# Performance work log

Measured on AMD Instinct MI355X. Metric: run time of the kernel, lower is better.

## Reference

```python
import jax, jax.numpy as jnp
import numpy as np
import math

H = W = 512
N_ANGLES = 180
TOTAL_ANGLES = 180.0
DIAG = int(math.ceil(math.sqrt(2.0) * max(H, W)))  # 725
PW = (DIAG - W) // 2  # 106
PH = (DIAG - H) // 2  # 106
P = W + 2 * PW        # 724 (torch F.pad arithmetic)


def setup_inputs() -> dict:
    key = jax.random.key(0)
    x = jax.random.normal(key, (H, W), dtype=jnp.float32)
    return {"x": x}


def _bilinear_sample_zeros(img, ix, iy):
    """grid_sample(align_corners=False, padding_mode='zeros') on a single [P,P] img.
    ix, iy: [N,P,P] pixel-space sample coords. Returns [N,P,P]."""
    n = img.shape[0]
    x0 = jnp.floor(ix)
    y0 = jnp.floor(iy)
    wx = ix - x0
    wy = iy - y0
    x0i = x0.astype(jnp.int32)
    y0i = y0.astype(jnp.int32)
    x1i = x0i + 1
    y1i = y0i + 1

    def g(yi, xi):
        v = img[jnp.clip(yi, 0, n - 1), jnp.clip(xi, 0, n - 1)]
        m = (yi >= 0) & (yi < n) & (xi >= 0) & (xi < n)
        return v * m.astype(img.dtype)

    return (g(y0i, x0i) * (1 - wx) * (1 - wy)
            + g(y0i, x1i) * wx * (1 - wy)
            + g(y1i, x0i) * (1 - wx) * wy
            + g(y1i, x1i) * wx * wy)


def reference(x):
    # pad image to (near-)diagonal square, matching torch F.pad semantics
    padded = jnp.pad(x, ((PH, PH), (PW, PW)))  # [P, P]

    angles_deg = jnp.linspace(0.0, TOTAL_ANGLES, N_ANGLES)
    ang = angles_deg * (jnp.pi / 180.0)
    c = jnp.cos(ang)[:, None, None]
    s = jnp.sin(ang)[:, None, None]

    # affine_grid normalized coords, align_corners=False: t = (2k+1)/P - 1
    t = (2.0 * jnp.arange(P, dtype=jnp.float32) + 1.0) / P - 1.0
    Xn = t[None, None, :]  # output x (width)
    Yn = t[None, :, None]  # output y (height)

    # theta = [[cos, -sin, 0],[sin, cos, 0]]
    xs = c * Xn - s * Yn   # [N,P,P] normalized sample x
    ys = s * Xn + c * Yn

    # unnormalize (align_corners=False)
    ix = ((xs + 1.0) * P - 1.0) * 0.5
    iy = ((ys + 1.0) * P - 1.0) * 0.5

    rotated = _bilinear_sample_zeros(padded, ix, iy)  # [N,P,P]
    # sinogram = rotated.squeeze(1).sum(dim=2) -> sum over last (width) axis
    sinogram = rotated.sum(axis=2)  # [N, P]
    return sinogram, rotated[:, None, :, :]
```

## Files before the change

kernel.cpp:

```cpp
#include <hip/hip_runtime.h>
#include <math.h>

#define N_ANGLES 180
#define P 724
#define W_IN 512

typedef float vfloat4 __attribute__((ext_vector_type(4)));

__global__ __launch_bounds__(256) void prep_all(const float* __restrict__ in,
                                                float* __restrict__ outT,
                                                float2* __restrict__ sc) {
    __shared__ float tile[32][33];
    const int bx = blockIdx.x * 32, by = blockIdx.y * 32;
    const int tx = threadIdx.x, ty = threadIdx.y;

    if (bx == 0 && by == 0) {
        int t = ty * 32 + tx;
        if (t < N_ANGLES) {
            float deg = (float)t * (180.0f / 179.0f);
            float ang = deg * (float)(M_PI / 180.0);
            sc[t] = make_float2(cosf(ang), sinf(ang));
        }
    }

    #pragma unroll
    for (int r = 0; r < 32; r += 8)
        tile[ty + r][tx] = in[(by + ty + r) * W_IN + bx + tx];
    __syncthreads();
    #pragma unroll
    for (int r = 0; r < 32; r += 8)
        outT[(bx + ty + r) * W_IN + by + tx] = tile[tx][ty + r];
}

template <int MODE>
__global__ __launch_bounds__(192) void radon_kernel(
    const float* __restrict__ x,
    const float2* __restrict__ sc,
    const float* __restrict__ xT,
    float* __restrict__ sino,
    float* __restrict__ rot)
{
    const int block = blockIdx.x;
    const int a = block / P;
    const int i = block - a * P;
    const int tid = threadIdx.x;

    float c, s;
    if (MODE > 0) {
        float2 cs = sc[a];
        c = cs.x; s = cs.y;
    } else {
        float deg = (float)a * (180.0f / 179.0f);
        float ang = deg * (float)(M_PI / 180.0);
        c = cosf(ang); s = sinf(ang);
    }

    const float fi = (float)i - 361.5f;
    const float Kx = 255.5f - 361.5f * c - s * fi;
    const float Ky = 255.5f - 361.5f * s + c * fi;

    const bool useT = (MODE == 2) && (fabsf(s) > fabsf(c));
    const float* __restrict__ bimg = useT ? xT : x;
    const float fcoef = useT ? s : c;
    const float fK    = useT ? Ky : Kx;
    const float scoef = useT ? c : s;
    const float sK    = useT ? Kx : Ky;

    float lo = 0.0f, hi = 723.0f;
    bool empty = false;
    {
        if (fabsf(c) >= 1e-3f) {
            float rc = 1.0f / c;
            float b1 = (-1.0f - Kx) * rc, b2 = (512.0f - Kx) * rc;
            lo = fmaxf(lo, fminf(b1, b2)); hi = fminf(hi, fmaxf(b1, b2));
        } else if (Kx <= -1.0f || Kx >= 512.0f) empty = true;
        if (fabsf(s) >= 1e-3f) {
            float rs = 1.0f / s;
            float b1 = (-1.0f - Ky) * rs, b2 = (512.0f - Ky) * rs;
            lo = fmaxf(lo, fminf(b1, b2)); hi = fminf(hi, fmaxf(b1, b2));
        } else if (Ky <= -1.0f || Ky >= 512.0f) empty = true;
    }
    int jlo, jhi;
    if (empty || lo > hi) { jlo = 1; jhi = 0; }
    else {
        jlo = max(0, (int)floorf(lo) - 2);
        jhi = min(723, (int)ceilf(hi) + 2);
    }

    float* rrow = rot + (size_t)block * P;
    float lsum = 0.0f;

    if (tid < 181) {
        const int j0 = tid << 2;
        vfloat4 o;
        if (j0 + 3 < jlo || j0 > jhi) {
            o = (vfloat4){0.0f, 0.0f, 0.0f, 0.0f};
        } else {
            const float jf = (float)j0;
            float fcv[4], scv[4];
            fcv[0] = fmaf(jf, fcoef, fK);
            scv[0] = fmaf(jf, scoef, sK);
            #pragma unroll
            for (int d = 1; d < 4; ++d) { fcv[d] = fcv[d-1] + fcoef; scv[d] = scv[d-1] + scoef; }

            float f0f[4], s0f[4];
            int f0i[4], s0i[4];
            bool interior = true;
            #pragma unroll
            for (int d = 0; d < 4; ++d) {
                f0f[d] = floorf(fcv[d]); s0f[d] = floorf(scv[d]);
                f0i[d] = (int)f0f[d];    s0i[d] = (int)s0f[d];
                interior = interior && ((unsigned)f0i[d] < 511u) && ((unsigned)s0i[d] < 511u);
            }

            float v[4];
            if (__all((int)interior)) {
                #pragma unroll
                for (int d = 0; d < 4; ++d) {
                    const float wf1 = fcv[d] - f0f[d], wf0 = 1.0f - wf1;
                    const float ws1 = scv[d] - s0f[d], ws0 = 1.0f - ws1;
                    const float* bp = bimg + (s0i[d] << 9) + f0i[d];
                    const float v00 = bp[0],   vA = bp[1];
                    const float vB  = bp[512], v11 = bp[513];
                    v[d] = fmaf(ws1, fmaf(wf1, v11, wf0 * vB),
                                ws0 * fmaf(wf1, vA, wf0 * v00));
                }
            } else {
                #pragma unroll
                for (int d = 0; d < 4; ++d) {
                    const int fa = f0i[d], fb = fa + 1;
                    const int sa = s0i[d], sb = sa + 1;
                    float wf1 = fcv[d] - f0f[d], wf0 = 1.0f - wf1;
                    float ws1 = scv[d] - s0f[d], ws0 = 1.0f - ws1;
                    wf0 = ((unsigned)fa < 512u) ? wf0 : 0.0f;
                    wf1 = ((unsigned)fb < 512u) ? wf1 : 0.0f;
                    ws0 = ((unsigned)sa < 512u) ? ws0 : 0.0f;
                    ws1 = ((unsigned)sb < 512u) ? ws1 : 0.0f;
                    const int fca = min(max(fa, 0), 511);
                    const int fcb = min(max(fb, 0), 511);
                    const int sca = min(max(sa, 0), 511);
                    const int scb = min(max(sb, 0), 511);
                    const float v00 = bimg[(sca << 9) + fca];
                    const float v01 = bimg[(sca << 9) + fcb];
                    const float v10 = bimg[(scb << 9) + fca];
                    const float v11 = bimg[(scb << 9) + fcb];
                    v[d] = fmaf(ws1, fmaf(wf1, v11, wf0 * v10),
                                ws0 * fmaf(wf1, v01, wf0 * v00));
                }
            }
            o = (vfloat4){v[0], v[1], v[2], v[3]};
        }
        __builtin_nontemporal_store(o, (vfloat4*)(rrow + j0));
        lsum = (o.x + o.y) + (o.z + o.w);
    }

    for (int off = 32; off > 0; off >>= 1)
        lsum += __shfl_down(lsum, off, 64);

    __shared__ float ws_red[3];
    const int lane = tid & 63;
    const int wid  = tid >> 6;
    if (lane == 0) ws_red[wid] = lsum;
    __syncthreads();
    if (tid == 0)
        sino[block] = ws_red[0] + ws_red[1] + ws_red[2];
}


extern "C" void kernel_launch(void* const* d_in, const int* in_sizes, int n_in,
                              void* d_out, int out_size, void* d_ws, size_t ws_size,
                              hipStream_t stream) {
    const float* x = (const float*)d_in[0];
    float* sino = (float*)d_out;
    float* rot  = sino + (size_t)N_ANGLES * P;
    float* ws   = (float*)d_ws;

    const dim3 grid(N_ANGLES * P), blk(192);
    if (ws && ws_size >= (size_t)(512 + 512 * 512) * sizeof(float)) {
        float* xT = ws + 512;
        prep_all<<<dim3(16, 16), dim3(32, 8), 0, stream>>>(x, xT, (float2*)ws);
        radon_kernel<2><<<grid, blk, 0, stream>>>(x, (const float2*)ws, xT, sino, rot);
    } else if (ws && ws_size >= (size_t)512 * sizeof(float)) {
        prep_all<<<dim3(16, 16), dim3(32, 8), 0, stream>>>(x, nullptr, (float2*)ws);
        radon_kernel<1><<<grid, blk, 0, stream>>>(x, (const float2*)ws, nullptr, sino, rot);
    } else {
        radon_kernel<0><<<grid, blk, 0, stream>>>(x, nullptr, nullptr, sino, rot);
    }
}
```

Baseline: 513.0 us.

## Process 4 output rows per block with 16x4 wavefront tiles over columns

Each block now covers four output rows of one angle instead of a single row. Each wavefront holds a 4-row by 16-column patch, so its gathered samples cluster in 2D for better cache locality. Threads step across columns in strides of 64 with incremental coordinates. The precomputed per-row valid column range is replaced by a per-iteration wave-level __any liveness check. Stores become scalar nontemporal stores instead of float4, and the row sum uses a 16-lane shuffle plus a small shared reduction, which may cost store efficiency.

```diff
diff --git a/kernel.cpp b/kernel.cpp
--- a/kernel.cpp
+++ b/kernel.cpp
@@ -4,8 +4,6 @@
 #define N_ANGLES 180
 #define P 724
 #define W_IN 512
-
-typedef float vfloat4 __attribute__((ext_vector_type(4)));
 
 __global__ __launch_bounds__(256) void prep_all(const float* __restrict__ in,
                                                 float* __restrict__ outT,
@@ -33,17 +31,21 @@
 }
 
 template <int MODE>
-__global__ __launch_bounds__(192) void radon_kernel(
+__global__ __launch_bounds__(256) void radon_kernel(
     const float* __restrict__ x,
     const float2* __restrict__ sc,
     const float* __restrict__ xT,
     float* __restrict__ sino,
     float* __restrict__ rot)
 {
-    const int block = blockIdx.x;
-    const int a = block / P;
-    const int i = block - a * P;
+    const int a  = blockIdx.y;
+    const int i0 = blockIdx.x << 2;
     const int tid = threadIdx.x;
+    const int w  = tid >> 6;
+    const int l  = tid & 63;
+    const int il = l >> 4;
+    const int jl = l & 15;
+    const int i  = i0 + il;
 
     float c, s;
     if (MODE > 0) {
@@ -62,108 +64,71 @@
     const bool useT = (MODE == 2) && (fabsf(s) > fabsf(c));
     const float* __restrict__ bimg = useT ? xT : x;
     const float fcoef = useT ? s : c;
+    const float scoef = useT ? c : s;
     const float fK    = useT ? Ky : Kx;
-    const float scoef = useT ? c : s;
     const float sK    = useT ? Kx : Ky;
 
-    float lo = 0.0f, hi = 723.0f;
-    bool empty = false;
-    {
-        if (fabsf(c) >= 1e-3f) {
-            float rc = 1.0f / c;
-            float b1 = (-1.0f - Kx) * rc, b2 = (512.0f - Kx) * rc;
-            lo = fmaxf(lo, fminf(b1, b2)); hi = fminf(hi, fmaxf(b1, b2));
-        } else if (Kx <= -1.0f || Kx >= 512.0f) empty = true;
-        if (fabsf(s) >= 1e-3f) {
-            float rs = 1.0f / s;
-            float b1 = (-1.0f - Ky) * rs, b2 = (512.0f - Ky) * rs;
-            lo = fmaxf(lo, fminf(b1, b2)); hi = fminf(hi, fmaxf(b1, b2));
-        } else if (Ky <= -1.0f || Ky >= 512.0f) empty = true;
-    }
-    int jlo, jhi;
-    if (empty || lo > hi) { jlo = 1; jhi = 0; }
-    else {
-        jlo = max(0, (int)floorf(lo) - 2);
-        jhi = min(723, (int)ceilf(hi) + 2);
+    const int jbase = (w << 4) + jl;
+    float fcv = fmaf((float)jbase, fcoef, fK);
+    float scv = fmaf((float)jbase, scoef, sK);
+    const float fstep = 64.0f * fcoef;
+    const float sstep = 64.0f * scoef;
+
+    float* __restrict__ rbase = rot + (size_t)(a * P + i) * P;
+    float lsum = 0.0f;
+
+    for (int it = 0; it < 12; ++it) {
+        const int j = jbase + (it << 6);
+        const bool valid = (j < P);
+        const bool live = valid && (fcv > -1.0f) && (fcv < 512.0f)
+                                && (scv > -1.0f) && (scv < 512.0f);
+        float val = 0.0f;
+        if (__any((int)live)) {
+            const float f0f = floorf(fcv), s0f = floorf(scv);
+            const int f0 = (int)f0f, s0 = (int)s0f;
+            const float wf1 = fcv - f0f, wf0 = 1.0f - wf1;
+            const float ws1 = scv - s0f, ws0 = 1.0f - ws1;
+            const bool inter = live && ((unsigned)f0 < 511u) && ((unsigned)s0 < 511u);
+            if (__all((int)inter)) {
+                const float* bp = bimg + (s0 << 9) + f0;
+                const float v00 = bp[0],   vA  = bp[1];
+                const float vB  = bp[512], v11 = bp[513];
+                val = fmaf(ws1, fmaf(wf1, v11, wf0 * vB),
+                           ws0 * fmaf(wf1, vA, wf0 * v00));
+            } else {
+                const int fb = f0 + 1, sb = s0 + 1;
+                const float a0 = ((unsigned)f0 < 512u) ? wf0 : 0.0f;
+                const float a1 = ((unsigned)fb < 512u) ? wf1 : 0.0f;
+                const float b0 = ((unsigned)s0 < 512u) ? ws0 : 0.0f;
+                const float b1 = ((unsigned)sb < 512u) ? ws1 : 0.0f;
+                const int fca = min(max(f0, 0), 511);
+                const int fcb = min(max(fb, 0), 511);
+                const int sca = min(max(s0, 0), 511);
+                const int scb = min(max(sb, 0), 511);
+                const float v00 = bimg[(sca << 9) + fca];
+                const float v01 = bimg[(sca << 9) + fcb];
+                const float v10 = bimg[(scb << 9) + fca];
+                const float v11 = bimg[(scb << 9) + fcb];
+                val = fmaf(b1, fmaf(a1, v11, a0 * v10),
+                           b0 * fmaf(a1, v01, a0 * v00));
+            }
+        }
+        if (valid) {
+            __builtin_nontemporal_store(val, rbase + j);
+            lsum += val;
+        }
+        fcv += fstep;
+        scv += sstep;
     }
 
-    float* rrow = rot + (size_t)block * P;
-    float lsum = 0.0f;
+    for (int off = 8; off > 0; off >>= 1)
+        lsum += __shfl_down(lsum, off, 16);
 
-    if (tid < 181) {
-        const int j0 = tid << 2;
-        vfloat4 o;
-        if (j0 + 3 < jlo || j0 > jhi) {
-            o = (vfloat4){0.0f, 0.0f, 0.0f, 0.0f};
-        } else {
-            const float jf = (float)j0;
-            float fcv[4], scv[4];
-            fcv[0] = fmaf(jf, fcoef, fK);
-            scv[0] = fmaf(jf, scoef, sK);
-            #pragma unroll
-            for (int d = 1; d < 4; ++d) { fcv[d] = fcv[d-1] + fcoef; scv[d] = scv[d-1] + scoef; }
-
-            float f0f[4], s0f[4];
-            int f0i[4], s0i[4];
-            bool interior = true;
-            #pragma unroll
-            for (int d = 0; d < 4; ++d) {
-                f0f[d] = floorf(fcv[d]); s0f[d] = floorf(scv[d]);
-                f0i[d] = (int)f0f[d];    s0i[d] = (int)s0f[d];
-                interior = interior && ((unsigned)f0i[d] < 511u) && ((unsigned)s0i[d] < 511u);
-            }
-
-            float v[4];
-            if (__all((int)interior)) {
-                #pragma unroll
-                for (int d = 0; d < 4; ++d) {
-                    const float wf1 = fcv[d] - f0f[d], wf0 = 1.0f - wf1;
-                    const float ws1 = scv[d] - s0f[d], ws0 = 1.0f - ws1;
-                    const float* bp = bimg + (s0i[d] << 9) + f0i[d];
-                    const float v00 = bp[0],   vA = bp[1];
-                    const float vB  = bp[512], v11 = bp[513];
-                    v[d] = fmaf(ws1, fmaf(wf1, v11, wf0 * vB),
-                                ws0 * fmaf(wf1, vA, wf0 * v00));
-                }
-            } else {
-                #pragma unroll
-                for (int d = 0; d < 4; ++d) {
-                    const int fa = f0i[d], fb = fa + 1;
-                    const int sa = s0i[d], sb = sa + 1;
-                    float wf1 = fcv[d] - f0f[d], wf0 = 1.0f - wf1;
-                    float ws1 = scv[d] - s0f[d], ws0 = 1.0f - ws1;
-                    wf0 = ((unsigned)fa < 512u) ? wf0 : 0.0f;
-                    wf1 = ((unsigned)fb < 512u) ? wf1 : 0.0f;
-                    ws0 = ((unsigned)sa < 512u) ? ws0 : 0.0f;
-                    ws1 = ((unsigned)sb < 512u) ? ws1 : 0.0f;
-                    const int fca = min(max(fa, 0), 511);
-                    const int fcb = min(max(fb, 0), 511);
-                    const int sca = min(max(sa, 0), 511);
-                    const int scb = min(max(sb, 0), 511);
-                    const float v00 = bimg[(sca << 9) + fca];
-                    const float v01 = bimg[(sca << 9) + fcb];
-                    const float v10 = bimg[(scb << 9) + fca];
-                    const float v11 = bimg[(scb << 9) + fcb];
-                    v[d] = fmaf(ws1, fmaf(wf1, v11, wf0 * v10),
-                                ws0 * fmaf(wf1, v01, wf0 * v00));
-                }
-            }
-            o = (vfloat4){v[0], v[1], v[2], v[3]};
-        }
-        __builtin_nontemporal_store(o, (vfloat4*)(rrow + j0));
-        lsum = (o.x + o.y) + (o.z + o.w);
-    }
-
-    for (int off = 32; off > 0; off >>= 1)
-        lsum += __shfl_down(lsum, off, 64);
-
-    __shared__ float ws_red[3];
-    const int lane = tid & 63;
-    const int wid  = tid >> 6;
-    if (lane == 0) ws_red[wid] = lsum;
+    __shared__ float red[16];
+    if (jl == 0) red[(w << 2) | il] = lsum;
     __syncthreads();
-    if (tid == 0)
-        sino[block] = ws_red[0] + ws_red[1] + ws_red[2];
+    if (tid < 4)
+        sino[a * P + i0 + tid] = red[tid] + red[4 + tid] + red[8 + tid] + red[12 + tid];
 }
 
 
@@ -175,7 +140,7 @@
     float* rot  = sino + (size_t)N_ANGLES * P;
     float* ws   = (float*)d_ws;
 
-    const dim3 grid(N_ANGLES * P), blk(192);
+    const dim3 grid(P / 4, N_ANGLES), blk(256);
     if (ws && ws_size >= (size_t)(512 + 512 * 512) * sizeof(float)) {
         float* xT = ws + 512;
         prep_all<<<dim3(16, 16), dim3(32, 8), 0, stream>>>(x, xT, (float2*)ws);
```

Result: slower. 560.9 us (+9.3%).
